# Performance work log

Hardware: AMD Instinct MI355X
Metric: run time of the kernel (lower is better)

The kernel has to match this reference:

```python
import jax, jax.numpy as jnp
import numpy as np

NUM_HEADS = 16
ROPE_THETA = 10000.0


def setup_inputs() -> dict:
    key = jax.random.key(0)
    k1, k2, k3 = jax.random.split(key, 3)
    B, T, C = 2, 2048, 1024
    x = jax.random.normal(k1, (B, T, C), dtype=jnp.float32)
    w_qkv = jax.random.normal(k2, (3 * C, C), dtype=jnp.float32) * 0.02
    w_out = jax.random.normal(k3, (C, C), dtype=jnp.float32) * 0.02
    return {"x": x, "w_qkv": w_qkv, "w_out": w_out}


def _apply_rope(x, cos, sin):
    # x: (B, H, T, D); interleaved complex pairs: (x[...,2i], x[...,2i+1])
    B, H, T, D = x.shape
    xp = x.reshape(B, H, T, D // 2, 2)
    xr, xi = xp[..., 0], xp[..., 1]
    # cos/sin: (T, D//2) broadcast over (B, H)
    out_r = xr * cos - xi * sin
    out_i = xr * sin + xi * cos
    return jnp.stack([out_r, out_i], axis=-1).reshape(B, H, T, D)


def reference(x, w_qkv, w_out):
    B, T, C = x.shape
    H = NUM_HEADS
    D = C // H
    scale = 1.0 / np.sqrt(D).astype(np.float32)

    qkv = x @ w_qkv.T                      # (B, T, 3C)
    q, k, v = jnp.split(qkv, 3, axis=-1)

    def to_heads(t):
        return t.reshape(B, T, H, D).transpose(0, 2, 1, 3)  # (B, H, T, D)

    q, k, v = to_heads(q), to_heads(k), to_heads(v)

    # RoPE frequencies: freqs[t, j] = t / theta^(2j/D)
    inv_freq = 1.0 / (ROPE_THETA ** (jnp.arange(0, D, 2, dtype=jnp.float32) / D))
    freqs = jnp.arange(T, dtype=jnp.float32)[:, None] * inv_freq[None, :]  # (T, D//2)
    cos, sin = jnp.cos(freqs), jnp.sin(freqs)

    q = _apply_rope(q, cos, sin)
    k = _apply_rope(k, cos, sin)

    att = jnp.einsum('bhqd,bhkd->bhqk', q, k) * scale   # (B, H, T, T)
    causal = jnp.tril(jnp.ones((T, T), dtype=bool))
    att = jnp.where(causal[None, None], att, -jnp.inf)
    att = jax.nn.softmax(att, axis=-1)
    # dropout p=0.0 (eval) -> identity

    out = jnp.einsum('bhqk,bhkd->bhqd', att, v)          # (B, H, T, D)
    out = out.transpose(0, 2, 1, 3).reshape(B, T, C)
    return out @ w_out.T
```

## Files before the change

### kernel.cpp

```cpp
#include <hip/hip_runtime.h>
#include <hip/hip_bf16.h>
#include <math.h>

#define DEV __device__ __forceinline__

typedef float  floatx4 __attribute__((ext_vector_type(4)));
typedef short  bf16x8  __attribute__((ext_vector_type(8)));
typedef short  bf16x4  __attribute__((ext_vector_type(4)));

typedef __attribute__((address_space(1))) void gvoid;
typedef __attribute__((address_space(3))) void lvoid;

static constexpr int Bc = 2, Tc = 2048, Cc = 1024, Hc = 16, Dc = 64;

DEV void gload16(const void* g, void* l) {
    __builtin_amdgcn_global_load_lds((gvoid*)g, (lvoid*)l, 16, 0, 0);
}

__global__ void prep_kernel(const float* __restrict__ xf,
                            const float* __restrict__ wqkvf,
                            const float* __restrict__ woutf,
                            __hip_bfloat16* __restrict__ xb,
                            __hip_bfloat16* __restrict__ wqkvb,
                            __hip_bfloat16* __restrict__ woutb,
                            float* __restrict__ cosT, float* __restrict__ sinT) {
    int gb = blockIdx.x;
    if (gb < 8192) {
        const float* src; __hip_bfloat16* dst; int i;
        if (gb < 4096)      { src = xf;    dst = xb;    i = gb * 256 + threadIdx.x; }
        else if (gb < 7168) { src = wqkvf; dst = wqkvb; i = (gb - 4096) * 256 + threadIdx.x; }
        else                { src = woutf; dst = woutb; i = (gb - 7168) * 256 + threadIdx.x; }
        float4 f = ((const float4*)src)[i];
        union { ushort4 u; __hip_bfloat16 h[4]; } pk;
        pk.h[0] = __float2bfloat16(f.x);
        pk.h[1] = __float2bfloat16(f.y);
        pk.h[2] = __float2bfloat16(f.z);
        pk.h[3] = __float2bfloat16(f.w);
        ((ushort4*)dst)[i] = pk.u;
    } else {
        int i = (gb - 8192) * 256 + threadIdx.x;
        int j = i >> 11, t = i & 2047;
        float invf = powf(10000.0f, -(float)j / 32.0f);
        float f = (float)t * invf;
        cosT[i] = cosf(f);
        sinT[i] = sinf(f);
    }
}

__global__ __launch_bounds__(256, 2) void gemm_qkv(
    const __hip_bfloat16* __restrict__ A,
    const __hip_bfloat16* __restrict__ Bm,
    __hip_bfloat16* __restrict__ qb,
    __hip_bfloat16* __restrict__ kb,
    __hip_bfloat16* __restrict__ vb,
    const float* __restrict__ cosT,
    const float* __restrict__ sinT,
    int K)
{
    __shared__ __align__(16) __hip_bfloat16 SM[2 * 128 * 64];
    __hip_bfloat16* const As = SM;
    __hip_bfloat16* const Bs = SM + 128 * 64;

    const int tid  = threadIdx.x;
    const int lane = tid & 63, wave = tid >> 6;
    const int quad = lane >> 4, cidx = lane & 15;
    const int wm = wave & 1, wn = wave >> 1;
    const int bm = blockIdx.x * 128, bn = blockIdx.y * 128;

    floatx4 acc[4][4] = {};

    for (int k0 = 0; k0 < K; k0 += 64) {
#pragma unroll
        for (int it = 0; it < 4; ++it) {
            int idx = tid + it * 256;
            int r = idx >> 3, cs = idx & 7;
            int cg = cs ^ (r & 7);
            gload16(A  + (size_t)(bm + r) * K + k0 + cg * 8, As + idx * 8);
            gload16(Bm + (size_t)(bn + r) * K + k0 + cg * 8, Bs + idx * 8);
        }
        __syncthreads();
#pragma unroll
        for (int ks = 0; ks < 2; ++ks) {
            bf16x8 af[4], bf[4];
#pragma unroll
            for (int mt = 0; mt < 4; ++mt) {
                int r = wm * 64 + mt * 16 + cidx;
                af[mt] = *(const bf16x8*)(As + (r * 8 + ((ks * 4 + quad) ^ (r & 7))) * 8);
            }
#pragma unroll
            for (int nt = 0; nt < 4; ++nt) {
                int r = wn * 64 + nt * 16 + cidx;
                bf[nt] = *(const bf16x8*)(Bs + (r * 8 + ((ks * 4 + quad) ^ (r & 7))) * 8);
            }
#pragma unroll
            for (int mt = 0; mt < 4; ++mt)
#pragma unroll
                for (int nt = 0; nt < 4; ++nt)
                    acc[mt][nt] = __builtin_amdgcn_mfma_f32_16x16x32_bf16(
                        af[mt], bf[nt], acc[mt][nt], 0, 0, 0);
        }
        __syncthreads();
    }

    if (bn >= 2048) {
#pragma unroll
        for (int nt = 0; nt < 4; ++nt) {
            int n_l = wn * 64 + nt * 16 + cidx;
#pragma unroll
            for (int mt = 0; mt < 4; ++mt)
#pragma unroll
                for (int reg = 0; reg < 4; ++reg) {
                    int m_l = wm * 64 + mt * 16 + quad * 4 + reg;
                    SM[n_l * 128 + (((m_l >> 3) ^ (n_l & 15)) * 8) + (m_l & 7)] =
                        __float2bfloat16(acc[mt][nt][reg]);
                }
        }
        __syncthreads();
        {
            int b = bm >> 11, t0 = bm & 2047;
            int c = tid & 15;
#pragma unroll
            for (int it = 0; it < 8; ++it) {
                int row = it * 16 + (tid >> 4);
                int cc = (bn - 2048) + row;
                int h = cc >> 6, d = cc & 63;
                *(uint4*)(vb + ((size_t)(b * Hc + h) * Dc + d) * Tc + t0 + c * 8) =
                    *(const uint4*)(SM + row * 128 + ((c ^ (row & 15)) * 8));
            }
        }
    } else {
        const float SL2E = 0.125f * 1.44269504088896f;
        const bool isq = (bn < 1024);
#pragma unroll
        for (int nt = 0; nt < 4; ++nt) {
            int n_l = wn * 64 + nt * 16 + cidx;
            int d = n_l & 63, j = d >> 1;
            const float* cp = cosT + j * 2048;
            const float* sp = sinT + j * 2048;
#pragma unroll
            for (int mt = 0; mt < 4; ++mt) {
                int m0 = wm * 64 + mt * 16 + quad * 4;
                int t0 = (bm + m0) & 2047;
                float4 c4 = *(const float4*)(cp + t0);
                float4 s4 = *(const float4*)(sp + t0);
#pragma unroll
                for (int reg = 0; reg < 4; ++reg) {
                    float v = acc[mt][nt][reg];
                    float p = __shfl_xor(v, 1);
                    float cz = ((const float*)&c4)[reg];
                    float sz = ((const float*)&s4)[reg];
                    float o = (d & 1) ? (p * sz + v * cz) : (v * cz - p * sz);
                    if (isq) o *= SL2E;
                    int m_l = m0 + reg;
                    SM[m_l * 128 + (((n_l >> 3) ^ (m_l & 15)) * 8) + (n_l & 7)] =
                        __float2bfloat16(o);
                }
            }
        }
        __syncthreads();
        {
            __hip_bfloat16* dst = isq ? qb : kb;
            const int bnl = bn & 1023;
#pragma unroll
            for (int it = 0; it < 8; ++it) {
                int c = it * 256 + tid;
                int row = c >> 4, s = c & 15;
                int m = bm + row;
                int b = m >> 11, t = m & 2047;
                int h = (bnl >> 6) + (s >> 3);
                int d0 = (s & 7) * 8;
                *(uint4*)(dst + ((size_t)(b * Hc + h) * Tc + t) * Dc + d0) =
                    *(const uint4*)(SM + row * 128 + ((s ^ (row & 15)) * 8));
            }
        }
    }
}

__global__ __launch_bounds__(256, 2) void gemm_out(
    const __hip_bfloat16* __restrict__ A,
    const __hip_bfloat16* __restrict__ Bm,
    float* __restrict__ Cout)
{
    __shared__ __align__(16) __hip_bfloat16 As[64 * 64];
    __shared__ __align__(16) __hip_bfloat16 Bs[128 * 64];

    const int tid  = threadIdx.x;
    const int lane = tid & 63, wave = tid >> 6;
    const int quad = lane >> 4, cidx = lane & 15;
    const int bm = blockIdx.x * 64, bn = blockIdx.y * 128;
    const int K = 1024;

    floatx4 acc[4][2] = {};

    for (int k0 = 0; k0 < K; k0 += 64) {
        int h = k0 >> 6;
#pragma unroll
        for (int it = 0; it < 2; ++it) {
            int idx = tid + it * 256;
            int r = idx >> 3, cs = idx & 7;
            int cg = cs ^ (r & 7);
            int m = bm + r;
            const __hip_bfloat16* src =
                A + ((size_t)((m >> 11) * 16 + h) * 2048 + (m & 2047)) * 64 + cg * 8;
            gload16(src, As + idx * 8);
        }
#pragma unroll
        for (int it = 0; it < 4; ++it) {
            int idx = tid + it * 256;
            int r = idx >> 3, cs = idx & 7;
            int cg = cs ^ (r & 7);
            gload16(Bm + (size_t)(bn + r) * K + k0 + cg * 8, Bs + idx * 8);
        }
        __syncthreads();
#pragma unroll
        for (int ks = 0; ks < 2; ++ks) {
            bf16x8 af[4], bf[2];
#pragma unroll
            for (int mt = 0; mt < 4; ++mt) {
                int r = mt * 16 + cidx;
                af[mt] = *(const bf16x8*)(As + (r * 8 + ((ks * 4 + quad) ^ (r & 7))) * 8);
            }
#pragma unroll
            for (int nt = 0; nt < 2; ++nt) {
                int r = wave * 32 + nt * 16 + cidx;
                bf[nt] = *(const bf16x8*)(Bs + (r * 8 + ((ks * 4 + quad) ^ (r & 7))) * 8);
            }
#pragma unroll
            for (int mt = 0; mt < 4; ++mt)
#pragma unroll
                for (int nt = 0; nt < 2; ++nt)
                    acc[mt][nt] = __builtin_amdgcn_mfma_f32_16x16x32_bf16(
                        af[mt], bf[nt], acc[mt][nt], 0, 0, 0);
        }
        __syncthreads();
    }

#pragma unroll
    for (int mt = 0; mt < 4; ++mt)
#pragma unroll
        for (int nt = 0; nt < 2; ++nt) {
            int n = bn + wave * 32 + nt * 16 + cidx;
#pragma unroll
            for (int reg = 0; reg < 4; ++reg) {
                int m = bm + mt * 16 + quad * 4 + reg;
                Cout[(size_t)m * 1024 + n] = acc[mt][nt][reg];
            }
        }
}

__global__ __launch_bounds__(256, 2) void attn_kernel(
    const __hip_bfloat16* __restrict__ qb,
    const __hip_bfloat16* __restrict__ kb,
    const __hip_bfloat16* __restrict__ vb,
    __hip_bfloat16* __restrict__ ob)
{
    __shared__ __align__(16) __hip_bfloat16 Kb[2 * 128 * 64];
    __shared__ __align__(16) __hip_bfloat16 Vb[2 * 64 * 128];
    __shared__ __align__(16) __hip_bfloat16 Os[64 * 64];

    const int tid  = threadIdx.x;
    const int lane = tid & 63, wave = tid >> 6;
    const int quad = lane >> 4, cidx = lane & 15;
    const int id = blockIdx.x;
    const int xcd = id & 7, s = id >> 3;
    const int bh = xcd * 4 + (s >> 4);
    const int bx = s & 15;
    const size_t plane = (size_t)bh * Tc * Dc;
    const __hip_bfloat16* Vp = vb + plane;
    const __hip_bfloat16* Kp = kb + plane;

    for (int half = 0; half < 2; ++half) {
        const int qt = half ? bx : 31 - bx;
        const int qbase = qt * 64;
        const int ktmax = (qbase + 63) >> 7;

#pragma unroll
        for (int it = 0; it < 2; ++it) {
            int idx = tid + it * 256;
            int r = idx >> 3, cg = (idx & 7) ^ (r & 7);
            gload16(qb + plane + (size_t)(qbase + r) * 64 + cg * 8, Os + idx * 8);
        }
#pragma unroll
        for (int it = 0; it < 4; ++it) {
            int idx = tid + it * 256;
            int r = idx >> 3, cg = (idx & 7) ^ (r & 7);
            gload16(Kp + (size_t)r * 64 + cg * 8, Kb + idx * 8);
        }
#pragma unroll
        for (int it = 0; it < 4; ++it) {
            int idx = tid + it * 256;
            int r = idx >> 4, c = (idx & 15) ^ (r & 15);
            gload16(Vp + (size_t)r * Tc + c * 8, Vb + idx * 8);
        }
        __syncthreads();

        bf16x8 qf[2];
#pragma unroll
        for (int ks = 0; ks < 2; ++ks) {
            int r = wave * 16 + cidx;
            qf[ks] = *(const bf16x8*)(Os + (r * 8 + ((ks * 4 + quad) ^ (r & 7))) * 8);
        }

        floatx4 oaccT[4] = {};
        float lsum = 0.0f;
        const int q = qbase + wave * 16 + cidx;

        for (int kt = 0; kt <= ktmax; ++kt) {
            const __hip_bfloat16* Kc = Kb + (kt & 1) * (128 * 64);
            const __hip_bfloat16* Vc = Vb + (kt & 1) * (64 * 128);

            if (kt < ktmax) {
                __hip_bfloat16* Kn = Kb + ((kt + 1) & 1) * (128 * 64);
                __hip_bfloat16* Vn = Vb + ((kt + 1) & 1) * (64 * 128);
#pragma unroll
                for (int it = 0; it < 4; ++it) {
                    int idx = tid + it * 256;
                    int r = idx >> 3, cg = (idx & 7) ^ (r & 7);
                    gload16(Kp + (size_t)((kt + 1) * 128 + r) * 64 + cg * 8, Kn + idx * 8);
                }
#pragma unroll
                for (int it = 0; it < 4; ++it) {
                    int idx = tid + it * 256;
                    int r = idx >> 4, c = (idx & 15) ^ (r & 15);
                    gload16(Vp + (size_t)r * Tc + (kt + 1) * 128 + c * 8, Vn + idx * 8);
                }
            }

            floatx4 sacc[8] = {};
#pragma unroll
            for (int ks = 0; ks < 2; ++ks)
#pragma unroll
                for (int kb2 = 0; kb2 < 8; ++kb2) {
                    int r = kb2 * 16 + cidx;
                    bf16x8 af = *(const bf16x8*)(
                        Kc + (r * 8 + ((ks * 4 + quad) ^ (r & 7))) * 8);
                    sacc[kb2] = __builtin_amdgcn_mfma_f32_16x16x32_bf16(
                        af, qf[ks], sacc[kb2], 0, 0, 0);
                }

            const bool domask = (kt == ktmax);
            bf16x4 pf[8];
#pragma unroll
            for (int kb2 = 0; kb2 < 8; ++kb2) {
#pragma unroll
                for (int reg = 0; reg < 4; ++reg) {
                    int key = kt * 128 + kb2 * 16 + quad * 4 + reg;
                    float p = __builtin_amdgcn_exp2f(sacc[kb2][reg]);
                    if (domask && key > q) p = 0.0f;
                    lsum += p;
                    __hip_bfloat16 hb = __float2bfloat16(p);
                    pf[kb2][reg] = *(const short*)&hb;
                }
            }

#pragma unroll
            for (int dt = 0; dt < 4; ++dt) {
                int d = dt * 16 + cidx;
#pragma unroll
                for (int c8 = 0; c8 < 8; ++c8) {
                    int ch = c8 * 2 + (quad >> 1);
                    bf16x4 vtf = *(const bf16x4*)(
                        Vc + (d * 16 + (ch ^ (d & 15))) * 8 + (quad & 1) * 4);
                    oaccT[dt] = __builtin_amdgcn_mfma_f32_16x16x16bf16_1k(
                        vtf, pf[c8], oaccT[dt], 0, 0, 0);
                }
            }

            __syncthreads();
        }

        float l = lsum;
        l += __shfl_xor(l, 16);
        l += __shfl_xor(l, 32);
        float inv = 1.0f / l;
        {
            int qq = wave * 16 + cidx;
#pragma unroll
            for (int dt = 0; dt < 4; ++dt) {
                bf16x4 o4;
#pragma unroll
                for (int reg = 0; reg < 4; ++reg) {
                    __hip_bfloat16 hb = __float2bfloat16(oaccT[dt][reg] * inv);
                    o4[reg] = *(const short*)&hb;
                }
                int g = dt * 4 + quad;
                *(bf16x4*)(Os + qq * 64 + ((g ^ (qq & 12)) * 4)) = o4;
            }
        }
        __syncthreads();
#pragma unroll
        for (int i = 0; i < 2; ++i) {
            int c = tid * 2 + i;
            int row = c >> 3, cp = c & 7;
            *(uint4*)(ob + plane + (size_t)(qbase + row) * 64 + cp * 8) =
                *(const uint4*)(Os + row * 64 + ((cp * 2) ^ (row & 12)) * 4);
        }
        __syncthreads();
    }
}

extern "C" void kernel_launch(void* const* d_in, const int* in_sizes, int n_in,
                              void* d_out, int out_size, void* d_ws, size_t ws_size,
                              hipStream_t stream) {
    const float* xf = nullptr; const float* wqkvf = nullptr; const float* woutf = nullptr;
    for (int i = 0; i < n_in; ++i) {
        if      (in_sizes[i] == 2 * 2048 * 1024) xf    = (const float*)d_in[i];
        else if (in_sizes[i] == 3 * 1024 * 1024) wqkvf = (const float*)d_in[i];
        else if (in_sizes[i] == 1024 * 1024)     woutf = (const float*)d_in[i];
    }
    float* out = (float*)d_out;

    char* ws = (char*)d_ws;
    const size_t MB = 1024 * 1024;
    __hip_bfloat16* qb    = (__hip_bfloat16*)(ws);
    __hip_bfloat16* kb    = (__hip_bfloat16*)(ws + 8  * MB);
    __hip_bfloat16* vb    = (__hip_bfloat16*)(ws + 16 * MB);
    __hip_bfloat16* ab    = (__hip_bfloat16*)(ws + 24 * MB);
    float* cosT           = (float*)(ws + 32 * MB);
    float* sinT           = (float*)(ws + 32 * MB + 256 * 1024);
    __hip_bfloat16* xb    = (__hip_bfloat16*)(ws + 33 * MB);
    __hip_bfloat16* wqkvb = (__hip_bfloat16*)(ws + 41 * MB);
    __hip_bfloat16* woutb = (__hip_bfloat16*)(ws + 47 * MB);

    prep_kernel<<<dim3(8448), dim3(256), 0, stream>>>(
        xf, wqkvf, woutf, xb, wqkvb, woutb, cosT, sinT);

    gemm_qkv<<<dim3(32, 24), dim3(256), 0, stream>>>(
        xb, wqkvb, qb, kb, vb, cosT, sinT, 1024);
    attn_kernel<<<dim3(512), dim3(256), 0, stream>>>(qb, kb, vb, ab);
    gemm_out<<<dim3(64, 8), dim3(256), 0, stream>>>(ab, woutb, out);
}
```

Measured before the change: 166.7 us.

## Process 128-query tiles per attention block, sharing K/V fragments across two query sub-tiles

```diff
diff --git a/kernel.cpp b/kernel.cpp
--- a/kernel.cpp
+++ b/kernel.cpp
@@ -254,148 +254,157 @@
     const __hip_bfloat16* __restrict__ vb,
     __hip_bfloat16* __restrict__ ob)
 {
-    __shared__ __align__(16) __hip_bfloat16 Kb[2 * 128 * 64];
-    __shared__ __align__(16) __hip_bfloat16 Vb[2 * 64 * 128];
-    __shared__ __align__(16) __hip_bfloat16 Os[64 * 64];
+    __shared__ __align__(16) __hip_bfloat16 KB[2 * 128 * 64];
+    __shared__ __align__(16) __hip_bfloat16 VB[2 * 64 * 128];
 
     const int tid  = threadIdx.x;
     const int lane = tid & 63, wave = tid >> 6;
     const int quad = lane >> 4, cidx = lane & 15;
     const int id = blockIdx.x;
     const int xcd = id & 7, s = id >> 3;
-    const int bh = xcd * 4 + (s >> 4);
-    const int bx = s & 15;
+    const int bh  = xcd * 4 + (s & 3);
+    const int m   = s >> 2;
+    const int qt  = (m < 8) ? (15 - m) : (m - 8);
+    const int qbase = qt * 128;
+    const int ktmax = qt;
     const size_t plane = (size_t)bh * Tc * Dc;
     const __hip_bfloat16* Vp = vb + plane;
     const __hip_bfloat16* Kp = kb + plane;
 
-    for (int half = 0; half < 2; ++half) {
-        const int qt = half ? bx : 31 - bx;
-        const int qbase = qt * 64;
-        const int ktmax = (qbase + 63) >> 7;
-
-#pragma unroll
-        for (int it = 0; it < 2; ++it) {
-            int idx = tid + it * 256;
-            int r = idx >> 3, cg = (idx & 7) ^ (r & 7);
-            gload16(qb + plane + (size_t)(qbase + r) * 64 + cg * 8, Os + idx * 8);
-        }
-#pragma unroll
-        for (int it = 0; it < 4; ++it) {
-            int idx = tid + it * 256;
-            int r = idx >> 3, cg = (idx & 7) ^ (r & 7);
-            gload16(Kp + (size_t)r * 64 + cg * 8, Kb + idx * 8);
-        }
-#pragma unroll
-        for (int it = 0; it < 4; ++it) {
-            int idx = tid + it * 256;
-            int r = idx >> 4, c = (idx & 15) ^ (r & 15);
-            gload16(Vp + (size_t)r * Tc + c * 8, Vb + idx * 8);
-        }
-        __syncthreads();
-
-        bf16x8 qf[2];
+    __hip_bfloat16* const Qs = KB + 128 * 64;
+    __hip_bfloat16* const Os = KB;
+
+#pragma unroll
+    for (int it = 0; it < 4; ++it) {
+        int idx = tid + it * 256;
+        int r = idx >> 3, cg = (idx & 7) ^ (r & 7);
+        gload16(qb + plane + (size_t)(qbase + r) * 64 + cg * 8, Qs + idx * 8);
+    }
+#pragma unroll
+    for (int it = 0; it < 4; ++it) {
+        int idx = tid + it * 256;
+        int r = idx >> 3, cg = (idx & 7) ^ (r & 7);
+        gload16(Kp + (size_t)r * 64 + cg * 8, KB + idx * 8);
+    }
+#pragma unroll
+    for (int it = 0; it < 4; ++it) {
+        int idx = tid + it * 256;
+        int r = idx >> 4, c = (idx & 15) ^ (r & 15);
+        gload16(Vp + (size_t)r * Tc + c * 8, VB + idx * 8);
+    }
+    __syncthreads();
+
+    bf16x8 qf[2][2];
+#pragma unroll
+    for (int qb2 = 0; qb2 < 2; ++qb2)
 #pragma unroll
         for (int ks = 0; ks < 2; ++ks) {
-            int r = wave * 16 + cidx;
-            qf[ks] = *(const bf16x8*)(Os + (r * 8 + ((ks * 4 + quad) ^ (r & 7))) * 8);
-        }
-
-        floatx4 oaccT[4] = {};
-        float lsum = 0.0f;
-        const int q = qbase + wave * 16 + cidx;
-
-        for (int kt = 0; kt <= ktmax; ++kt) {
-            const __hip_bfloat16* Kc = Kb + (kt & 1) * (128 * 64);
-            const __hip_bfloat16* Vc = Vb + (kt & 1) * (64 * 128);
-
-            if (kt < ktmax) {
-                __hip_bfloat16* Kn = Kb + ((kt + 1) & 1) * (128 * 64);
-                __hip_bfloat16* Vn = Vb + ((kt + 1) & 1) * (64 * 128);
-#pragma unroll
-                for (int it = 0; it < 4; ++it) {
-                    int idx = tid + it * 256;
-                    int r = idx >> 3, cg = (idx & 7) ^ (r & 7);
-                    gload16(Kp + (size_t)((kt + 1) * 128 + r) * 64 + cg * 8, Kn + idx * 8);
+            int r = wave * 32 + qb2 * 16 + cidx;
+            qf[qb2][ks] = *(const bf16x8*)(Qs + (r * 8 + ((ks * 4 + quad) ^ (r & 7))) * 8);
+        }
+    __syncthreads();
+
+    floatx4 oaccT[2][4] = {};
+    floatx4 lpart[2] = {};
+    const int q0 = qbase + wave * 32 + cidx;
+
+    for (int kt = 0; kt <= ktmax; ++kt) {
+        const __hip_bfloat16* Kc = KB + (kt & 1) * (128 * 64);
+        const __hip_bfloat16* Vc = VB + (kt & 1) * (64 * 128);
+
+        if (kt < ktmax) {
+            __hip_bfloat16* Kn = KB + ((kt + 1) & 1) * (128 * 64);
+            __hip_bfloat16* Vn = VB + ((kt + 1) & 1) * (64 * 128);
+#pragma unroll
+            for (int it = 0; it < 4; ++it) {
+                int idx = tid + it * 256;
+                int r = idx >> 3, cg = (idx & 7) ^ (r & 7);
+                gload16(Kp + (size_t)((kt + 1) * 128 + r) * 64 + cg * 8, Kn + idx * 8);
+            }
+#pragma unroll
+            for (int it = 0; it < 4; ++it) {
+                int idx = tid + it * 256;
+                int r = idx >> 4, c = (idx & 15) ^ (r & 15);
+                gload16(Vp + (size_t)r * Tc + (kt + 1) * 128 + c * 8, Vn + idx * 8);
+            }
+        }
+
+        floatx4 sacc[2][8] = {};
+#pragma unroll
+        for (int ks = 0; ks < 2; ++ks)
+#pragma unroll
+            for (int kb8 = 0; kb8 < 8; ++kb8) {
+                int r = kb8 * 16 + cidx;
+                bf16x8 af = *(const bf16x8*)(
+                    Kc + (r * 8 + ((ks * 4 + quad) ^ (r & 7))) * 8);
+                sacc[0][kb8] = __builtin_amdgcn_mfma_f32_16x16x32_bf16(
+                    af, qf[0][ks], sacc[0][kb8], 0, 0, 0);
+                sacc[1][kb8] = __builtin_amdgcn_mfma_f32_16x16x32_bf16(
+                    af, qf[1][ks], sacc[1][kb8], 0, 0, 0);
+            }
+
+        const bool domask = (kt == ktmax);
+        bf16x4 pf[2][8];
+#pragma unroll
+        for (int qb2 = 0; qb2 < 2; ++qb2) {
+            const int q = q0 + qb2 * 16;
+#pragma unroll
+            for (int kb8 = 0; kb8 < 8; ++kb8)
+#pragma unroll
+                for (int reg = 0; reg < 4; ++reg) {
+                    int key = kt * 128 + kb8 * 16 + quad * 4 + reg;
+                    float p = __builtin_amdgcn_exp2f(sacc[qb2][kb8][reg]);
+                    if (domask && key > q) p = 0.0f;
+                    lpart[qb2][reg] += p;
+                    __hip_bfloat16 hb = __float2bfloat16(p);
+                    pf[qb2][kb8][reg] = *(const short*)&hb;
                 }
-#pragma unroll
-                for (int it = 0; it < 4; ++it) {
-                    int idx = tid + it * 256;
-                    int r = idx >> 4, c = (idx & 15) ^ (r & 15);
-                    gload16(Vp + (size_t)r * Tc + (kt + 1) * 128 + c * 8, Vn + idx * 8);
-                }
-            }
-
-            floatx4 sacc[8] = {};
-#pragma unroll
-            for (int ks = 0; ks < 2; ++ks)
-#pragma unroll
-                for (int kb2 = 0; kb2 < 8; ++kb2) {
-                    int r = kb2 * 16 + cidx;
-                    bf16x8 af = *(const bf16x8*)(
-                        Kc + (r * 8 + ((ks * 4 + quad) ^ (r & 7))) * 8);
-                    sacc[kb2] = __builtin_amdgcn_mfma_f32_16x16x32_bf16(
-                        af, qf[ks], sacc[kb2], 0, 0, 0);
-                }
-
-            const bool domask = (kt == ktmax);
-            bf16x4 pf[8];
-#pragma unroll
-            for (int kb2 = 0; kb2 < 8; ++kb2) {
-#pragma unroll
-                for (int reg = 0; reg < 4; ++reg) {
-                    int key = kt * 128 + kb2 * 16 + quad * 4 + reg;
-                    float p = __builtin_amdgcn_exp2f(sacc[kb2][reg]);
-                    if (domask && key > q) p = 0.0f;
-                    lsum += p;
-                    __hip_bfloat16 hb = __float2bfloat16(p);
-                    pf[kb2][reg] = *(const short*)&hb;
-                }
-            }
-
-#pragma unroll
-            for (int dt = 0; dt < 4; ++dt) {
-                int d = dt * 16 + cidx;
-#pragma unroll
-                for (int c8 = 0; c8 < 8; ++c8) {
-                    int ch = c8 * 2 + (quad >> 1);
-                    bf16x4 vtf = *(const bf16x4*)(
-                        Vc + (d * 16 + (ch ^ (d & 15))) * 8 + (quad & 1) * 4);
-                    oaccT[dt] = __builtin_amdgcn_mfma_f32_16x16x16bf16_1k(
-                        vtf, pf[c8], oaccT[dt], 0, 0, 0);
-                }
-            }
-
-            __syncthreads();
-        }
-
-        float l = lsum;
+        }
+
+#pragma unroll
+        for (int dt = 0; dt < 4; ++dt) {
+            int d = dt * 16 + cidx;
+#pragma unroll
+            for (int c8 = 0; c8 < 8; ++c8) {
+                int ch = c8 * 2 + (quad >> 1);
+                bf16x4 vtf = *(const bf16x4*)(
+                    Vc + (d * 16 + (ch ^ (d & 15))) * 8 + (quad & 1) * 4);
+                oaccT[0][dt] = __builtin_amdgcn_mfma_f32_16x16x16bf16_1k(
+                    vtf, pf[0][c8], oaccT[0][dt], 0, 0, 0);
+                oaccT[1][dt] = __builtin_amdgcn_mfma_f32_16x16x16bf16_1k(
+                    vtf, pf[1][c8], oaccT[1][dt], 0, 0, 0);
+            }
+        }
+
+        __syncthreads();
+    }
+
+#pragma unroll
+    for (int qb2 = 0; qb2 < 2; ++qb2) {
+        float l = lpart[qb2][0] + lpart[qb2][1] + lpart[qb2][2] + lpart[qb2][3];
         l += __shfl_xor(l, 16);
         l += __shfl_xor(l, 32);
         float inv = 1.0f / l;
-        {
-            int qq = wave * 16 + cidx;
-#pragma unroll
-            for (int dt = 0; dt < 4; ++dt) {
-                bf16x4 o4;
-#pragma unroll
-                for (int reg = 0; reg < 4; ++reg) {
-                    __hip_bfloat16 hb = __float2bfloat16(oaccT[dt][reg] * inv);
-                    o4[reg] = *(const short*)&hb;
-                }
-                int g = dt * 4 + quad;
-                *(bf16x4*)(Os + qq * 64 + ((g ^ (qq & 12)) * 4)) = o4;
-            }
-        }
-        __syncthreads();
-#pragma unroll
-        for (int i = 0; i < 2; ++i) {
-            int c = tid * 2 + i;
-            int row = c >> 3, cp = c & 7;
-            *(uint4*)(ob + plane + (size_t)(qbase + row) * 64 + cp * 8) =
-                *(const uint4*)(Os + row * 64 + ((cp * 2) ^ (row & 12)) * 4);
-        }
-        __syncthreads();
+        int qq = wave * 32 + qb2 * 16 + cidx;
+#pragma unroll
+        for (int dt = 0; dt < 4; ++dt) {
+            bf16x4 o4;
+#pragma unroll
+            for (int reg = 0; reg < 4; ++reg) {
+                __hip_bfloat16 hb = __float2bfloat16(oaccT[qb2][dt][reg] * inv);
+                o4[reg] = *(const short*)&hb;
+            }
+            int g = dt * 4 + quad;
+            *(bf16x4*)(Os + qq * 64 + ((g ^ (qq & 12)) * 4)) = o4;
+        }
+    }
+    __syncthreads();
+#pragma unroll
+    for (int i = 0; i < 4; ++i) {
+        int c = tid + i * 256;
+        int row = c >> 3, cp = c & 7;
+        *(uint4*)(ob + plane + (size_t)(qbase + row) * 64 + cp * 8) =
+            *(const uint4*)(Os + row * 64 + ((cp * 2) ^ (row & 12)) * 4);
     }
 }
 
```

After: 162.7 us. -2.4%, faster.
